# Kernel optimization log

Measured on AMD Instinct MI355X. Metric: run time of the kernel, lower is better.

The kernel has to match this reference:

```python
import jax, jax.numpy as jnp
import numpy as np

MODEL_DIM = 1024
NUM_EXPERTS = 64
CAPACITY_FACTOR = 1.0
MIN_CAPACITY = 8


def setup_inputs() -> dict:
    key = jax.random.key(0)
    kx, kw = jax.random.split(key)
    x = jax.random.normal(kx, (4, 2048, MODEL_DIM), dtype=jnp.float32)
    wg = jax.random.normal(kw, (MODEL_DIM, NUM_EXPERTS), dtype=jnp.float32) * (1.0 / np.sqrt(MODEL_DIM))
    return {"x": x, "wg": wg}


def reference(x, wg):
    d = x.shape[-1]
    tokens = x.reshape(-1, d)                      # [s, m]
    s = tokens.shape[0]
    e = wg.shape[1]
    # capacity per _capacity(): ceil(num_tokens/num_experts * capacity_factor), floored at min_capacity
    capacity = max(int(np.ceil(s / e * CAPACITY_FACTOR)), MIN_CAPACITY)

    logits = tokens @ wg                           # [s, e]  (wg Linear, no bias)
    gates = jax.nn.softmax(logits, axis=1)         # [s, e]

    indices1_s = jnp.argmax(gates, axis=1)         # [s] top-1 expert per token
    mask1 = jax.nn.one_hot(indices1_s, e, dtype=jnp.int32)  # [s, e]
    exp_counts = jnp.sum(mask1, axis=0)            # [e]

    # load-balancing aux loss
    me = jnp.mean(gates, axis=0)                   # [e]
    ce = jnp.mean(mask1.astype(jnp.float32), axis=0)
    l_aux = jnp.sum(me * ce) * e

    # position of each token within its expert's buffer
    locations1 = jnp.cumsum(mask1, axis=0) - 1     # [s, e]
    locations1_s = jnp.sum(locations1 * mask1, axis=1)  # [s]

    gates_masked = gates * mask1.astype(jnp.float32)    # [s, e]
    # one_hot zeros out indices >= capacity (token dropped)
    locations1_sc = jax.nn.one_hot(locations1_s, capacity, dtype=jnp.float32)  # [s, c]
    combine_weights = jnp.einsum('se,sc->sec', gates_masked, locations1_sc)    # [s, e, c]
    dispatch_mask = combine_weights.astype(bool)
    return (l_aux, combine_weights, dispatch_mask, mask1, exp_counts, indices1_s)
```

## Files before the change

### kernel.cpp

```cpp
#include <hip/hip_runtime.h>
#include <hip/hip_bf16.h>

#define S_TOK 8192
#define NEXP 64
#define MDIM 1024
#define CAP 128
#define NCH 512
#define CHUNK 16
#define DT 256
#define NPH 4

#define OFF2 67108865
#define OFF3 134217729
#define OFF4 134742017
#define OFF5 134742081

__global__ __launch_bounds__(256) void gate_kernel(
    const float* __restrict__ x, const float* __restrict__ wg,
    unsigned char* __restrict__ ind, unsigned char* __restrict__ rnk,
    float* __restrict__ gval, unsigned char* __restrict__ counts,
    float* __restrict__ gparts)
{
  __shared__ float wgt[DT * NEXP];
  __shared__ float g_all[CHUNK][NEXP];
  __shared__ int s_ind[CHUNK];
  const int b = blockIdx.x;
  const int tid = threadIdx.x;
  const int lane = tid & 63;
  const int wv = tid >> 6;
  const int lt = lane >> 4;
  const int eg = lane & 15;
  const int tk = b * CHUNK + wv * 4 + lt;

  const float4* x4 = reinterpret_cast<const float4*>(x);
  const float4* wg4 = reinterpret_cast<const float4*>(wg);
  float4* wl4 = reinterpret_cast<float4*>(wgt);

  float acc0 = 0.f, acc1 = 0.f, acc2 = 0.f, acc3 = 0.f;
#pragma unroll
  for (int p = 0; p < NPH; ++p) {
#pragma unroll
    for (int i = 0; i < DT * NEXP / 4 / 256; ++i)
      wl4[i * 256 + tid] = wg4[p * (DT * NEXP / 4) + i * 256 + tid];
    __syncthreads();

    const int xbase = tk * (MDIM / 4) + p * (DT / 4);
#pragma unroll 2
    for (int dq = 0; dq < DT / 4; ++dq) {
      const float4 xv = x4[xbase + dq];
      {
        const float4 w = wl4[(4 * dq + 0) * 16 + eg];
        acc0 = fmaf(xv.x, w.x, acc0); acc1 = fmaf(xv.x, w.y, acc1);
        acc2 = fmaf(xv.x, w.z, acc2); acc3 = fmaf(xv.x, w.w, acc3);
      }
      {
        const float4 w = wl4[(4 * dq + 1) * 16 + eg];
        acc0 = fmaf(xv.y, w.x, acc0); acc1 = fmaf(xv.y, w.y, acc1);
        acc2 = fmaf(xv.y, w.z, acc2); acc3 = fmaf(xv.y, w.w, acc3);
      }
      {
        const float4 w = wl4[(4 * dq + 2) * 16 + eg];
        acc0 = fmaf(xv.z, w.x, acc0); acc1 = fmaf(xv.z, w.y, acc1);
        acc2 = fmaf(xv.z, w.z, acc2); acc3 = fmaf(xv.z, w.w, acc3);
      }
      {
        const float4 w = wl4[(4 * dq + 3) * 16 + eg];
        acc0 = fmaf(xv.w, w.x, acc0); acc1 = fmaf(xv.w, w.y, acc1);
        acc2 = fmaf(xv.w, w.z, acc2); acc3 = fmaf(xv.w, w.w, acc3);
      }
    }
    __syncthreads();
  }

  float m = acc0; int ei = eg * 4;
  if (acc1 > m) { m = acc1; ei = eg * 4 + 1; }
  if (acc2 > m) { m = acc2; ei = eg * 4 + 2; }
  if (acc3 > m) { m = acc3; ei = eg * 4 + 3; }
#pragma unroll
  for (int off = 1; off <= 8; off <<= 1) {
    const float om = __shfl_xor(m, off, 64);
    const int oe = __shfl_xor(ei, off, 64);
    if (om > m || (om == m && oe < ei)) { m = om; ei = oe; }
  }
  const float e0 = __expf(acc0 - m), e1 = __expf(acc1 - m),
              e2 = __expf(acc2 - m), e3 = __expf(acc3 - m);
  float sm = e0 + e1 + e2 + e3;
#pragma unroll
  for (int off = 1; off <= 8; off <<= 1) sm += __shfl_xor(sm, off, 64);
  const float inv = 1.0f / sm;

  *reinterpret_cast<float4*>(&g_all[wv * 4 + lt][eg * 4]) =
      make_float4(e0 * inv, e1 * inv, e2 * inv, e3 * inv);
  if (eg == 0) {
    s_ind[wv * 4 + lt] = ei;
    ind[tk] = (unsigned char)ei;
    gval[tk] = inv;
  }
  __syncthreads();

  if (wv == 0) {
    float colsum = 0.f;
#pragma unroll
    for (int t = 0; t < CHUNK; ++t) colsum += g_all[t][lane];
    gparts[b * NEXP + lane] = colsum;
    int cnt = 0;
#pragma unroll
    for (int t = 0; t < CHUNK; ++t) {
      const int e = s_ind[t];
      const int r = __shfl(cnt, e, 64);
      if (lane == 0) rnk[b * CHUNK + t] = (unsigned char)r;
      cnt += (lane == e) ? 1 : 0;
    }
    counts[b * NEXP + lane] = (unsigned char)cnt;
  }
}

__global__ __launch_bounds__(1024) void reduce_kernel(
    const unsigned char* __restrict__ counts, const float* __restrict__ gparts,
    unsigned short* __restrict__ offs, float* __restrict__ out)
{
  __shared__ int s_cnt[16][64];
  __shared__ float s_gs[16][64];
  const int e = threadIdx.x & 63;
  const int g = threadIdx.x >> 6;
  const int ch0 = g * 32;

  int csum = 0; float gsum = 0.f;
#pragma unroll 8
  for (int ch = ch0; ch < ch0 + 32; ++ch) {
    csum += (int)counts[ch * NEXP + e];
    gsum += gparts[ch * NEXP + e];
  }
  s_cnt[g][e] = csum; s_gs[g][e] = gsum;
  __syncthreads();

  int base = 0;
  for (int k = 0; k < g; ++k) base += s_cnt[k][e];
  int run = base;
#pragma unroll 8
  for (int ch = ch0; ch < ch0 + 32; ++ch) {
    offs[ch * NEXP + e] = (unsigned short)run;
    run += (int)counts[ch * NEXP + e];
  }
  if (g == 15) {
    const int total = run;
    out[OFF4 + e] = (float)total;
    float gtot = 0.f;
#pragma unroll
    for (int k = 0; k < 16; ++k) gtot += s_gs[k][e];
    const float me = gtot * (1.0f / (float)S_TOK);
    const float ce = (float)total * (1.0f / (float)S_TOK);
    float prod = me * ce;
#pragma unroll
    for (int off = 32; off > 0; off >>= 1) prod += __shfl_xor(prod, off, 64);
    if (e == 0) out[0] = prod * (float)NEXP;
  }
}

__global__ __launch_bounds__(256) void scatter_kernel(
    const unsigned char* __restrict__ ind, const unsigned char* __restrict__ rnk,
    const unsigned short* __restrict__ offs, const float* __restrict__ gval,
    float* __restrict__ out)
{
  const int s = blockIdx.x * 256 + threadIdx.x;
  if (s >= S_TOK) return;
  const int e = (int)ind[s];
  const int loc = (int)offs[(s >> 4) * NEXP + e] + (int)rnk[s];
  out[OFF5 + s] = (float)e;
  out[OFF3 + (s << 6) + e] = 1.0f;
  if (loc < CAP) {
    const int rel = (s << 13) + (e << 7) + loc;
    out[1 + rel] = gval[s];
    out[OFF2 + rel] = 1.0f;
  }
}

extern "C" void kernel_launch(void* const* d_in, const int* in_sizes, int n_in,
                              void* d_out, int out_size, void* d_ws, size_t ws_size,
                              hipStream_t stream)
{
  const float* x = (const float*)d_in[0];
  const float* wg = (const float*)d_in[1];
  float* out = (float*)d_out;

  float* gval = (float*)d_ws;
  float* gparts = gval + S_TOK;
  unsigned short* offs = (unsigned short*)(gparts + NCH * NEXP);
  unsigned char* ind = (unsigned char*)(offs + NCH * NEXP);
  unsigned char* rnk = ind + S_TOK;
  unsigned char* counts = rnk + S_TOK;

  hipMemsetAsync(out, 0, (size_t)out_size * sizeof(float), stream);
  gate_kernel<<<NCH, 256, 0, stream>>>(x, wg, ind, rnk, gval, counts, gparts);
  reduce_kernel<<<1, 1024, 0, stream>>>(counts, gparts, offs, out);
  scatter_kernel<<<(S_TOK + 255) / 256, 256, 0, stream>>>(ind, rnk, offs, gval, out);
}
```

Baseline: 161.0 us.

## Fuse output zeroing into gate kernel to overlap memset with gating compute

Replaces the separate hipMemsetAsync of the large output buffer with zero-fill blocks launched in the same grid as the gate blocks. One in four of the first 2048 blocks computes gating, and the rest, plus the extra blocks beyond, zero float4 slabs of the output. The intent is to overlap the bandwidth-bound clear with the compute-bound gating matmul and drop one launch. It relies on hand-computed slab sizes and on block index interleaving to cover the whole output. Gate blocks that share the shared-memory allocation could lower occupancy for the zeroing blocks.

```diff
diff --git a/kernel.cpp b/kernel.cpp
--- a/kernel.cpp
+++ b/kernel.cpp
@@ -14,23 +14,42 @@
 #define OFF3 134217729
 #define OFF4 134742017
 #define OFF5 134742081
-
-__global__ __launch_bounds__(256) void gate_kernel(
+#define OUT_ELEMS 134750273
+#define SLOTS_TOT 33687568
+#define SLAB 16450
+#define GRID_MAIN 2560
+
+__global__ __launch_bounds__(256) void main_kernel(
     const float* __restrict__ x, const float* __restrict__ wg,
     unsigned char* __restrict__ ind, unsigned char* __restrict__ rnk,
     float* __restrict__ gval, unsigned char* __restrict__ counts,
-    float* __restrict__ gparts)
+    float* __restrict__ gparts, float* __restrict__ out)
 {
   __shared__ float wgt[DT * NEXP];
   __shared__ float g_all[CHUNK][NEXP];
   __shared__ int s_ind[CHUNK];
   const int b = blockIdx.x;
+  const bool isGate = (b < 2048) && ((b & 3) == 0);
+
+  if (!isGate) {
+    const int f = (b < 2048) ? (b - (b >> 2) - 1) : (b - 512);
+    const long long start = (long long)f * SLAB;
+    long long end = start + SLAB;
+    if (end > SLOTS_TOT) end = SLOTS_TOT;
+    float4* o4 = reinterpret_cast<float4*>(out);
+    const float4 z = make_float4(0.f, 0.f, 0.f, 0.f);
+    for (long long j = start + threadIdx.x; j < end; j += 256) o4[j] = z;
+    if (b == 1 && threadIdx.x == 0) out[OUT_ELEMS - 1] = 0.f;
+    return;
+  }
+
+  const int g = b >> 2;
   const int tid = threadIdx.x;
   const int lane = tid & 63;
   const int wv = tid >> 6;
   const int lt = lane >> 4;
   const int eg = lane & 15;
-  const int tk = b * CHUNK + wv * 4 + lt;
+  const int tk = g * CHUNK + wv * 4 + lt;
 
   const float4* x4 = reinterpret_cast<const float4*>(x);
   const float4* wg4 = reinterpret_cast<const float4*>(wg);
@@ -102,16 +121,16 @@
     float colsum = 0.f;
 #pragma unroll
     for (int t = 0; t < CHUNK; ++t) colsum += g_all[t][lane];
-    gparts[b * NEXP + lane] = colsum;
+    gparts[g * NEXP + lane] = colsum;
     int cnt = 0;
 #pragma unroll
     for (int t = 0; t < CHUNK; ++t) {
       const int e = s_ind[t];
       const int r = __shfl(cnt, e, 64);
-      if (lane == 0) rnk[b * CHUNK + t] = (unsigned char)r;
+      if (lane == 0) rnk[g * CHUNK + t] = (unsigned char)r;
       cnt += (lane == e) ? 1 : 0;
     }
-    counts[b * NEXP + lane] = (unsigned char)cnt;
+    counts[g * NEXP + lane] = (unsigned char)cnt;
   }
 }
 
@@ -190,8 +209,7 @@
   unsigned char* rnk = ind + S_TOK;
   unsigned char* counts = rnk + S_TOK;
 
-  hipMemsetAsync(out, 0, (size_t)out_size * sizeof(float), stream);
-  gate_kernel<<<NCH, 256, 0, stream>>>(x, wg, ind, rnk, gval, counts, gparts);
+  main_kernel<<<GRID_MAIN, 256, 0, stream>>>(x, wg, ind, rnk, gval, counts, gparts, out);
   reduce_kernel<<<1, 1024, 0, stream>>>(counts, gparts, offs, out);
   scatter_kernel<<<(S_TOK + 255) / 256, 256, 0, stream>>>(ind, rnk, offs, gval, out);
 }
```

Measured after the change: 297.4 us. 84.8% more time.

## Split K across waves with 8 tokens per thread and reduce partial logits in LDS

Applied to the files above, without the earlier changes.

The gate GEMM is reorganised so each block handles 32 tokens. Each wave takes a quarter of the model dimension, and each thread accumulates 8 tokens × 4 experts, so every weight read from LDS is reused across 8 tokens instead of 1. Partial logits are then reduced across waves through shared memory before the softmax and argmax. Blocks drop from 512 to 256, and the reduce and scatter kernels are adjusted to the new chunk size. This raises register pressure and lowers grid parallelism, and x loads become strided across tokens.

```diff
diff --git a/kernel.cpp b/kernel.cpp
--- a/kernel.cpp
+++ b/kernel.cpp
@@ -5,10 +5,8 @@
 #define NEXP 64
 #define MDIM 1024
 #define CAP 128
-#define NCH 512
-#define CHUNK 16
-#define DT 256
-#define NPH 4
+#define BLK_TOK 32
+#define NCH 256
 
 #define OFF2 67108865
 #define OFF3 134217729
@@ -21,94 +19,113 @@
     float* __restrict__ gval, unsigned char* __restrict__ counts,
     float* __restrict__ gparts)
 {
-  __shared__ float wgt[DT * NEXP];
-  __shared__ float g_all[CHUNK][NEXP];
-  __shared__ int s_ind[CHUNK];
+  __shared__ float wgt[4 * 64 * NEXP];
+  __shared__ float g_all[BLK_TOK][NEXP];
+  __shared__ int s_ind[BLK_TOK];
   const int b = blockIdx.x;
   const int tid = threadIdx.x;
   const int lane = tid & 63;
   const int wv = tid >> 6;
-  const int lt = lane >> 4;
   const int eg = lane & 15;
-  const int tk = b * CHUNK + wv * 4 + lt;
+  const int tg = lane >> 4;
+  const int tokbase = b * BLK_TOK + tg * 8;
 
   const float4* x4 = reinterpret_cast<const float4*>(x);
   const float4* wg4 = reinterpret_cast<const float4*>(wg);
-  float4* wl4 = reinterpret_cast<float4*>(wgt);
-
-  float acc0 = 0.f, acc1 = 0.f, acc2 = 0.f, acc3 = 0.f;
-#pragma unroll
-  for (int p = 0; p < NPH; ++p) {
-#pragma unroll
-    for (int i = 0; i < DT * NEXP / 4 / 256; ++i)
-      wl4[i * 256 + tid] = wg4[p * (DT * NEXP / 4) + i * 256 + tid];
+  float4* wgt4 = reinterpret_cast<float4*>(wgt);
+
+  float4 acc[8];
+#pragma unroll
+  for (int j = 0; j < 8; ++j) acc[j] = make_float4(0.f, 0.f, 0.f, 0.f);
+
+#pragma unroll
+  for (int p = 0; p < 4; ++p) {
     __syncthreads();
-
-    const int xbase = tk * (MDIM / 4) + p * (DT / 4);
+#pragma unroll
+    for (int k = 0; k < 16; ++k) {
+      const int c = k * 256 + tid;
+      const int wq = c >> 10;
+      const int rem = c & 1023;
+      wgt4[c] = wg4[wq * 4096 + p * 1024 + rem];
+    }
+    __syncthreads();
+
+    const float4* wrow = wgt4 + wv * 1024;
+    const int xcol0 = wv * 64 + p * 16;
 #pragma unroll 2
-    for (int dq = 0; dq < DT / 4; ++dq) {
-      const float4 xv = x4[xbase + dq];
-      {
-        const float4 w = wl4[(4 * dq + 0) * 16 + eg];
-        acc0 = fmaf(xv.x, w.x, acc0); acc1 = fmaf(xv.x, w.y, acc1);
-        acc2 = fmaf(xv.x, w.z, acc2); acc3 = fmaf(xv.x, w.w, acc3);
+    for (int dq = 0; dq < 16; ++dq) {
+      const float4 w0 = wrow[(4 * dq + 0) * 16 + eg];
+      const float4 w1 = wrow[(4 * dq + 1) * 16 + eg];
+      const float4 w2 = wrow[(4 * dq + 2) * 16 + eg];
+      const float4 w3 = wrow[(4 * dq + 3) * 16 + eg];
+#pragma unroll
+      for (int j = 0; j < 8; ++j) {
+        const float4 xv = x4[(tokbase + j) * (MDIM / 4) + xcol0 + dq];
+        acc[j].x = fmaf(xv.x, w0.x, fmaf(xv.y, w1.x, fmaf(xv.z, w2.x, fmaf(xv.w, w3.x, acc[j].x))));
+        acc[j].y = fmaf(xv.x, w0.y, fmaf(xv.y, w1.y, fmaf(xv.z, w2.y, fmaf(xv.w, w3.y, acc[j].y))));
+        acc[j].z = fmaf(xv.x, w0.z, fmaf(xv.y, w1.z, fmaf(xv.z, w2.z, fmaf(xv.w, w3.z, acc[j].z))));
+        acc[j].w = fmaf(xv.x, w0.w, fmaf(xv.y, w1.w, fmaf(xv.z, w2.w, fmaf(xv.w, w3.w, acc[j].w))));
       }
-      {
-        const float4 w = wl4[(4 * dq + 1) * 16 + eg];
-        acc0 = fmaf(xv.y, w.x, acc0); acc1 = fmaf(xv.y, w.y, acc1);
-        acc2 = fmaf(xv.y, w.z, acc2); acc3 = fmaf(xv.y, w.w, acc3);
-      }
-      {
-        const float4 w = wl4[(4 * dq + 2) * 16 + eg];
-        acc0 = fmaf(xv.z, w.x, acc0); acc1 = fmaf(xv.z, w.y, acc1);
-        acc2 = fmaf(xv.z, w.z, acc2); acc3 = fmaf(xv.z, w.w, acc3);
-      }
-      {
-        const float4 w = wl4[(4 * dq + 3) * 16 + eg];
-        acc0 = fmaf(xv.w, w.x, acc0); acc1 = fmaf(xv.w, w.y, acc1);
-        acc2 = fmaf(xv.w, w.z, acc2); acc3 = fmaf(xv.w, w.w, acc3);
-      }
-    }
-    __syncthreads();
-  }
-
-  float m = acc0; int ei = eg * 4;
-  if (acc1 > m) { m = acc1; ei = eg * 4 + 1; }
-  if (acc2 > m) { m = acc2; ei = eg * 4 + 2; }
-  if (acc3 > m) { m = acc3; ei = eg * 4 + 3; }
-#pragma unroll
-  for (int off = 1; off <= 8; off <<= 1) {
-    const float om = __shfl_xor(m, off, 64);
-    const int oe = __shfl_xor(ei, off, 64);
-    if (om > m || (om == m && oe < ei)) { m = om; ei = oe; }
-  }
-  const float e0 = __expf(acc0 - m), e1 = __expf(acc1 - m),
-              e2 = __expf(acc2 - m), e3 = __expf(acc3 - m);
-  float sm = e0 + e1 + e2 + e3;
-#pragma unroll
-  for (int off = 1; off <= 8; off <<= 1) sm += __shfl_xor(sm, off, 64);
-  const float inv = 1.0f / sm;
-
-  *reinterpret_cast<float4*>(&g_all[wv * 4 + lt][eg * 4]) =
-      make_float4(e0 * inv, e1 * inv, e2 * inv, e3 * inv);
-  if (eg == 0) {
-    s_ind[wv * 4 + lt] = ei;
-    ind[tk] = (unsigned char)ei;
-    gval[tk] = inv;
+    }
+  }
+
+  __syncthreads();
+#pragma unroll
+  for (int j = 0; j < 8; ++j)
+    wgt4[(wv * BLK_TOK + tg * 8 + j) * 16 + eg] = acc[j];
+  __syncthreads();
+
+#pragma unroll
+  for (int jj = 0; jj < 2; ++jj) {
+    const int tl = wv * 8 + jj * 4 + tg;
+    const float4 s0 = wgt4[(0 * BLK_TOK + tl) * 16 + eg];
+    const float4 s1 = wgt4[(1 * BLK_TOK + tl) * 16 + eg];
+    const float4 s2 = wgt4[(2 * BLK_TOK + tl) * 16 + eg];
+    const float4 s3 = wgt4[(3 * BLK_TOK + tl) * 16 + eg];
+    const float l0 = s0.x + s1.x + s2.x + s3.x;
+    const float l1 = s0.y + s1.y + s2.y + s3.y;
+    const float l2 = s0.z + s1.z + s2.z + s3.z;
+    const float l3 = s0.w + s1.w + s2.w + s3.w;
+
+    float m = l0; int ei = eg * 4;
+    if (l1 > m) { m = l1; ei = eg * 4 + 1; }
+    if (l2 > m) { m = l2; ei = eg * 4 + 2; }
+    if (l3 > m) { m = l3; ei = eg * 4 + 3; }
+#pragma unroll
+    for (int off = 1; off <= 8; off <<= 1) {
+      const float om = __shfl_xor(m, off, 64);
+      const int oe = __shfl_xor(ei, off, 64);
+      if (om > m || (om == m && oe < ei)) { m = om; ei = oe; }
+    }
+    const float e0 = __expf(l0 - m), e1 = __expf(l1 - m),
+                e2 = __expf(l2 - m), e3 = __expf(l3 - m);
+    float sm = e0 + e1 + e2 + e3;
+#pragma unroll
+    for (int off = 1; off <= 8; off <<= 1) sm += __shfl_xor(sm, off, 64);
+    const float inv = 1.0f / sm;
+
+    *reinterpret_cast<float4*>(&g_all[tl][eg * 4]) =
+        make_float4(e0 * inv, e1 * inv, e2 * inv, e3 * inv);
+    if (eg == 0) {
+      s_ind[tl] = ei;
+      const int gt = b * BLK_TOK + tl;
+      ind[gt] = (unsigned char)ei;
+      gval[gt] = inv;
+    }
   }
   __syncthreads();
 
   if (wv == 0) {
     float colsum = 0.f;
 #pragma unroll
-    for (int t = 0; t < CHUNK; ++t) colsum += g_all[t][lane];
+    for (int t = 0; t < BLK_TOK; ++t) colsum += g_all[t][lane];
     gparts[b * NEXP + lane] = colsum;
     int cnt = 0;
 #pragma unroll
-    for (int t = 0; t < CHUNK; ++t) {
+    for (int t = 0; t < BLK_TOK; ++t) {
       const int e = s_ind[t];
       const int r = __shfl(cnt, e, 64);
-      if (lane == 0) rnk[b * CHUNK + t] = (unsigned char)r;
+      if (lane == 0) rnk[b * BLK_TOK + t] = (unsigned char)r;
       cnt += (lane == e) ? 1 : 0;
     }
     counts[b * NEXP + lane] = (unsigned char)cnt;
@@ -123,11 +140,11 @@
   __shared__ float s_gs[16][64];
   const int e = threadIdx.x & 63;
   const int g = threadIdx.x >> 6;
-  const int ch0 = g * 32;
+  const int ch0 = g * 16;
 
   int csum = 0; float gsum = 0.f;
-#pragma unroll 8
-  for (int ch = ch0; ch < ch0 + 32; ++ch) {
+#pragma unroll
+  for (int ch = ch0; ch < ch0 + 16; ++ch) {
     csum += (int)counts[ch * NEXP + e];
     gsum += gparts[ch * NEXP + e];
   }
@@ -137,8 +154,8 @@
   int base = 0;
   for (int k = 0; k < g; ++k) base += s_cnt[k][e];
   int run = base;
-#pragma unroll 8
-  for (int ch = ch0; ch < ch0 + 32; ++ch) {
+#pragma unroll
+  for (int ch = ch0; ch < ch0 + 16; ++ch) {
     offs[ch * NEXP + e] = (unsigned short)run;
     run += (int)counts[ch * NEXP + e];
   }
@@ -165,7 +182,7 @@
   const int s = blockIdx.x * 256 + threadIdx.x;
   if (s >= S_TOK) return;
   const int e = (int)ind[s];
-  const int loc = (int)offs[(s >> 4) * NEXP + e] + (int)rnk[s];
+  const int loc = (int)offs[(s >> 5) * NEXP + e] + (int)rnk[s];
   out[OFF5 + s] = (float)e;
   out[OFF3 + (s << 6) + e] = 1.0f;
   if (loc < CAP) {
```

New measurement: 134.5 us. 16.5% less time.
